# Performance work log

Measured on AMD Instinct MI355X. Metric: run time of the kernel, lower is better.

Reference implementation:

```python
import jax, jax.numpy as jnp
import numpy as np

L, H, C, D = 4, 4, 64, 64  # layers, heads, per-head out channels, embedding_dim
NEG_SLOPE = 0.2
LN_EPS = 1e-5

def layer_norm(x, g, b):
    mu = x.mean(-1, keepdims=True)
    var = ((x - mu) ** 2).mean(-1, keepdims=True)
    return (x - mu) * jax.lax.rsqrt(var + LN_EPS) * g + b

def setup_inputs() -> dict:
    key = jax.random.key(0)
    N, E = 20000, 320000
    ks = jax.random.split(key, 12)
    f = lambda k, shape: jax.random.normal(k, shape, jnp.float32) * 0.1
    return {
        "node_feats": jax.random.normal(ks[0], (N, D), jnp.float32),
        "edge_feats": jax.random.normal(ks[1], (E, D), jnp.float32),
        "edge_index": jax.random.randint(ks[2], (2, E), 0, N),
        "W_lin": f(ks[3], (L, D, H * C)),      # GAT node projection (bias=False)
        "W_edge": f(ks[4], (L, D, H * C)),     # GAT edge projection (bias=False)
        "att_src": f(ks[5], (L, H, C)),
        "att_dst": f(ks[6], (L, H, C)),
        "att_edge": f(ks[7], (L, H, C)),
        "bias_conv": f(ks[8], (L, D)),
        "ln_g": jnp.ones((L, D), jnp.float32),
        "ln_b": jnp.zeros((L, D), jnp.float32),
        "eW1": f(ks[9], (L, 3 * D, 3 * D)),
        "eb1": jnp.zeros((L, 3 * D), jnp.float32),
        "eln_g": jnp.ones((L, 3 * D), jnp.float32),
        "eln_b": jnp.zeros((L, 3 * D), jnp.float32),
        "eW2": f(ks[10], (L, 3 * D, D)),
        "eb2": jnp.zeros((L, D), jnp.float32),
    }

def reference(node_feats, edge_feats, edge_index, W_lin, W_edge, att_src,
              att_dst, att_edge, bias_conv, ln_g, ln_b, eW1, eb1, eln_g,
              eln_b, eW2, eb2):
    N = node_feats.shape[0]
    src, dst = edge_index[0], edge_index[1]
    for l in range(L):
        # --- GAT attention conv (concat=False: mean over heads) ---
        x = (node_feats @ W_lin[l]).reshape(N, H, C)
        e = (edge_feats @ W_edge[l]).reshape(-1, H, C)
        x_j, x_i = x[src], x[dst]                                  # [E,H,C]
        alpha = ((x_j * att_src[l]).sum(-1) + (x_i * att_dst[l]).sum(-1)
                 + (e * att_edge[l]).sum(-1))                      # [E,H]
        alpha = jax.nn.leaky_relu(alpha, NEG_SLOPE)
        amax = jax.ops.segment_max(alpha, dst, num_segments=N)
        alpha = jnp.exp(alpha - amax[dst])
        denom = jax.ops.segment_sum(alpha, dst, num_segments=N)
        alpha = alpha / (denom[dst] + 1e-16)
        out = jax.ops.segment_sum(x_j * alpha[..., None], dst, num_segments=N)
        out = out.mean(axis=1) + bias_conv[l]                      # [N,D]
        node_feats = layer_norm(out, ln_g[l], ln_b[l])
        # --- SparseEdgeUpdateLayer (residual=True) ---
        ni, nj = node_feats[src], node_feats[dst]
        h = jnp.concatenate([ni + nj, jnp.abs(ni - nj), edge_feats], axis=-1)
        h = jax.nn.relu(layer_norm(h @ eW1[l] + eb1[l], eln_g[l], eln_b[l]))
        edge_feats = h @ eW2[l] + eb2[l] + edge_feats
        # dropout is identity in eval mode
        if l < L - 1:
            node_feats = jax.nn.relu(node_feats)
    return node_feats, edge_feats
```

## Files before the change

kernel.cpp:

```cpp
#include <hip/hip_runtime.h>
#include <math.h>

#define NLAYERS 4
#define H 4
#define C 64
#define D 64
#define HC 256
#define D3 192
#define NEG 0.2f

typedef float f32x4 __attribute__((ext_vector_type(4)));
typedef short bf16x8 __attribute__((ext_vector_type(8)));
typedef unsigned short u16;

__device__ __forceinline__ u16 f2bf(float f) {
    unsigned u = __float_as_uint(f);
    u += 0x7FFFu + ((u >> 16) & 1u);
    return (u16)(u >> 16);
}
__device__ __forceinline__ float bf2f(u16 h) {
    return __uint_as_float((unsigned)h << 16);
}

__global__ void k_weffs(const float* __restrict__ W_edge, const float* __restrict__ att_edge,
                        const float* __restrict__ W_lin, const float* __restrict__ att_s,
                        const float* __restrict__ att_d,
                        float* __restrict__ weff, float* __restrict__ w_asd) {
    int l = blockIdx.x;
    const float* We = W_edge + (size_t)l * D * HC;
    const float* Wl = W_lin + (size_t)l * D * HC;
    const float* ae = att_edge + l * H * C;
    const float* as_ = att_s + l * H * C;
    const float* ad = att_d + l * H * C;
    int t = threadIdx.x;
    int d = t >> 2, h = t & 3;
    float se = 0.f, ss = 0.f, sd = 0.f;
    #pragma unroll
    for (int c = 0; c < C; ++c) {
        float we = We[d * HC + h * C + c];
        float wl = Wl[d * HC + h * C + c];
        se = fmaf(we, ae[h * C + c], se);
        ss = fmaf(wl, as_[h * C + c], ss);
        sd = fmaf(wl, ad[h * C + c], sd);
    }
    weff[l * HC + d * 4 + h] = se;
    w_asd[l * 512 + d * 8 + h] = ss;
    w_asd[l * 512 + d * 8 + 4 + h] = sd;
}

__global__ void k_cvtw(const float* __restrict__ W1, const float* __restrict__ W2,
                       u16* __restrict__ W1T, u16* __restrict__ W2T) {
    int i = blockIdx.x * 256 + threadIdx.x;
    if (i < NLAYERS * D3 * D3) {
        int l = i / (D3 * D3), r = i % (D3 * D3);
        int n = r / D3, k = r % D3;
        W1T[i] = f2bf(W1[l * D3 * D3 + k * D3 + n]);
    } else {
        int j = i - NLAYERS * D3 * D3;
        if (j < NLAYERS * D3 * D) {
            int l = j / (D3 * D), r = j % (D3 * D);
            int n = r / D3, k = r % D3;
            W2T[j] = f2bf(W2[l * D3 * D + k * D + n]);
        }
    }
}

__global__ void k_cvtwl(const float* __restrict__ W_lin,
                        u16* __restrict__ WTh, u16* __restrict__ WTl) {
    int i = blockIdx.x * 256 + threadIdx.x;
    if (i >= NLAYERS * HC * D) return;
    int l = i / (HC * D), r = i % (HC * D);
    int o = r / D, d = r % D;
    float v = W_lin[(size_t)l * D * HC + d * HC + o];
    u16 h = f2bf(v);
    WTh[i] = h;
    WTl[i] = f2bf(v - bf2f(h));
}

__global__ void k_hist(const int* __restrict__ dst, int* __restrict__ deg, int E) {
    int i = blockIdx.x * blockDim.x + threadIdx.x;
    if (i < E) atomicAdd(&deg[dst[i]], 1);
}

__global__ void k_scan(const int* __restrict__ deg, int* __restrict__ rowptr,
                       int* __restrict__ head, int N, int E) {
    __shared__ int lds[1024];
    int t = threadIdx.x;
    int chunk = (N + 1023) / 1024;
    int begin = t * chunk, end = min(begin + chunk, N);
    int sum = 0;
    for (int i = begin; i < end; ++i) sum += deg[i];
    lds[t] = sum;
    __syncthreads();
    for (int off = 1; off < 1024; off <<= 1) {
        int v = (t >= off) ? lds[t - off] : 0;
        __syncthreads();
        lds[t] += v;
        __syncthreads();
    }
    int running = (t == 0) ? 0 : lds[t - 1];
    for (int i = begin; i < end; ++i) {
        int dg = deg[i];
        rowptr[i] = running;
        head[i] = running;
        running += dg;
    }
    if (t == 0) rowptr[N] = E;
}

__global__ void k_scatter(const int* __restrict__ src, const int* __restrict__ dst,
                          int* __restrict__ head, int* __restrict__ csrpos,
                          int* __restrict__ perm_src, int E) {
    int i = blockIdx.x * blockDim.x + threadIdx.x;
    if (i < E) {
        int d = dst[i];
        int pos = atomicAdd(&head[d], 1);
        csrpos[i] = pos;
        perm_src[pos] = src[i];
    }
}

__global__ __launch_bounds__(256, 4) void k_nodeproj_mfma(
    const float* __restrict__ nf, const u16* __restrict__ WTh, const u16* __restrict__ WTl,
    const float* __restrict__ w_asd, float* __restrict__ x,
    float* __restrict__ a_src, float* __restrict__ a_dst, int N, int relu_in) {
    __shared__ __align__(16) u16 s_ah[32 * 72];
    __shared__ __align__(16) u16 s_al[32 * 72];
    __shared__ __align__(16) float s_nf[32][68];
    __shared__ __align__(16) float s_wasd[512];
    int tid = threadIdx.x;
    int w = tid >> 6, lane = tid & 63;
    int n0 = blockIdx.x << 5;

    if (tid < 128) *(float4*)&s_wasd[tid * 4] = *(const float4*)&w_asd[tid * 4];

    {
        int r = tid >> 3, c0 = (tid & 7) << 3;
        int n = n0 + r;
        float4 v0 = make_float4(0.f, 0.f, 0.f, 0.f), v1 = v0;
        if (n < N) {
            v0 = *(const float4*)&nf[(size_t)n * D + c0];
            v1 = *(const float4*)&nf[(size_t)n * D + c0 + 4];
        }
        if (relu_in) {
            v0.x = fmaxf(v0.x, 0.f); v0.y = fmaxf(v0.y, 0.f);
            v0.z = fmaxf(v0.z, 0.f); v0.w = fmaxf(v0.w, 0.f);
            v1.x = fmaxf(v1.x, 0.f); v1.y = fmaxf(v1.y, 0.f);
            v1.z = fmaxf(v1.z, 0.f); v1.w = fmaxf(v1.w, 0.f);
        }
        *(float4*)&s_nf[r][c0] = v0;
        *(float4*)&s_nf[r][c0 + 4] = v1;
        float vv[8] = {v0.x, v0.y, v0.z, v0.w, v1.x, v1.y, v1.z, v1.w};
        bf16x8 hv, lv;
        #pragma unroll
        for (int j = 0; j < 8; ++j) {
            u16 h = f2bf(vv[j]);
            hv[j] = (short)h;
            lv[j] = (short)f2bf(vv[j] - bf2f(h));
        }
        *(bf16x8*)&s_ah[r * 72 + c0] = hv;
        *(bf16x8*)&s_al[r * 72 + c0] = lv;
    }
    __syncthreads();

    int m16 = lane & 15, quad = lane >> 4, kq = quad * 8;
    f32x4 acc[2][4];
    #pragma unroll
    for (int mt = 0; mt < 2; ++mt)
        #pragma unroll
        for (int nt = 0; nt < 4; ++nt) {
            acc[mt][nt][0] = 0.f; acc[mt][nt][1] = 0.f;
            acc[mt][nt][2] = 0.f; acc[mt][nt][3] = 0.f;
        }
    #pragma unroll
    for (int ks = 0; ks < 2; ++ks) {
        int ko = ks * 32 + kq;
        bf16x8 ah0 = *(const bf16x8*)&s_ah[m16 * 72 + ko];
        bf16x8 ah1 = *(const bf16x8*)&s_ah[(16 + m16) * 72 + ko];
        bf16x8 al0 = *(const bf16x8*)&s_al[m16 * 72 + ko];
        bf16x8 al1 = *(const bf16x8*)&s_al[(16 + m16) * 72 + ko];
        #pragma unroll
        for (int nt = 0; nt < 4; ++nt) {
            int col = w * 64 + nt * 16 + m16;
            bf16x8 bh = *(const bf16x8*)&WTh[col * D + ko];
            bf16x8 bl = *(const bf16x8*)&WTl[col * D + ko];
            acc[0][nt] = __builtin_amdgcn_mfma_f32_16x16x32_bf16(ah0, bh, acc[0][nt], 0, 0, 0);
            acc[0][nt] = __builtin_amdgcn_mfma_f32_16x16x32_bf16(al0, bh, acc[0][nt], 0, 0, 0);
            acc[0][nt] = __builtin_amdgcn_mfma_f32_16x16x32_bf16(ah0, bl, acc[0][nt], 0, 0, 0);
            acc[1][nt] = __builtin_amdgcn_mfma_f32_16x16x32_bf16(ah1, bh, acc[1][nt], 0, 0, 0);
            acc[1][nt] = __builtin_amdgcn_mfma_f32_16x16x32_bf16(al1, bh, acc[1][nt], 0, 0, 0);
            acc[1][nt] = __builtin_amdgcn_mfma_f32_16x16x32_bf16(ah1, bl, acc[1][nt], 0, 0, 0);
        }
    }
    #pragma unroll
    for (int mt = 0; mt < 2; ++mt) {
        #pragma unroll
        for (int nt = 0; nt < 4; ++nt) {
            int col = w * 64 + nt * 16 + m16;
            #pragma unroll
            for (int r = 0; r < 4; ++r) {
                int n = n0 + mt * 16 + quad * 4 + r;
                if (n < N) x[(size_t)n * HC + col] = acc[mt][nt][r];
            }
        }
    }

    {
        int nloc = tid >> 3, o = tid & 7;
        float s = 0.f;
        #pragma unroll
        for (int d = 0; d < 64; ++d)
            s = fmaf(s_nf[nloc][d], s_wasd[d * 8 + o], s);
        int n = n0 + nloc;
        if (n < N) {
            if (o < 4) a_src[n * 4 + o] = s;
            else       a_dst[n * 4 + (o - 4)] = s;
        }
    }
}

__global__ void k_alpha(const float* __restrict__ ef, const float* __restrict__ weff,
                        const int* __restrict__ src, const int* __restrict__ dst,
                        const float* __restrict__ a_src, const float* __restrict__ a_dst,
                        const int* __restrict__ csrpos, float* __restrict__ alpha_csr, int E) {
    int wave = (int)((blockIdx.x * blockDim.x + threadIdx.x) >> 6);
    int lane = threadIdx.x & 63;
    int sub = lane >> 4, li = lane & 15;
    int e = wave * 4 + sub;
    if (e >= E) return;
    float4 efv = *(const float4*)&ef[(size_t)e * D + li * 4];
    float4 w0 = *(const float4*)&weff[(li * 4 + 0) * 4];
    float4 w1 = *(const float4*)&weff[(li * 4 + 1) * 4];
    float4 w2 = *(const float4*)&weff[(li * 4 + 2) * 4];
    float4 w3 = *(const float4*)&weff[(li * 4 + 3) * 4];
    float p0 = efv.x * w0.x + efv.y * w1.x + efv.z * w2.x + efv.w * w3.x;
    float p1 = efv.x * w0.y + efv.y * w1.y + efv.z * w2.y + efv.w * w3.y;
    float p2 = efv.x * w0.z + efv.y * w1.z + efv.z * w2.z + efv.w * w3.z;
    float p3 = efv.x * w0.w + efv.y * w1.w + efv.z * w2.w + efv.w * w3.w;
    #pragma unroll
    for (int off = 1; off < 16; off <<= 1) {
        p0 += __shfl_xor(p0, off);
        p1 += __shfl_xor(p1, off);
        p2 += __shfl_xor(p2, off);
        p3 += __shfl_xor(p3, off);
    }
    if (li < 4) {
        float p = (li == 0) ? p0 : (li == 1) ? p1 : (li == 2) ? p2 : p3;
        int s = src[e], dd = dst[e];
        float a = p + a_src[s * 4 + li] + a_dst[dd * 4 + li];
        a = (a > 0.f) ? a : NEG * a;
        alpha_csr[(size_t)csrpos[e] * 4 + li] = a;
    }
}

__global__ void k_gat(const float* __restrict__ x, float* __restrict__ alpha_csr,
                      const int* __restrict__ rowptr, const int* __restrict__ perm_src,
                      const float* __restrict__ bias, const float* __restrict__ g,
                      const float* __restrict__ b, float* __restrict__ nf_ln,
                      float* __restrict__ out2, int N) {
    int n = (int)((blockIdx.x * blockDim.x + threadIdx.x) >> 6);
    int lane = threadIdx.x & 63;
    if (n >= N) return;
    int s = rowptr[n], e = rowptr[n + 1];
    int deg = e - s;
    float m0 = -1e30f, m1 = -1e30f, m2 = -1e30f, m3 = -1e30f;
    for (int i = lane; i < deg; i += 64) {
        const float4 a = *(const float4*)&alpha_csr[(size_t)(s + i) * 4];
        m0 = fmaxf(m0, a.x); m1 = fmaxf(m1, a.y);
        m2 = fmaxf(m2, a.z); m3 = fmaxf(m3, a.w);
    }
    #pragma unroll
    for (int off = 32; off; off >>= 1) {
        m0 = fmaxf(m0, __shfl_xor(m0, off)); m1 = fmaxf(m1, __shfl_xor(m1, off));
        m2 = fmaxf(m2, __shfl_xor(m2, off)); m3 = fmaxf(m3, __shfl_xor(m3, off));
    }
    float d0 = 0.f, d1 = 0.f, d2 = 0.f, d3 = 0.f;
    for (int i = lane; i < deg; i += 64) {
        float4 a = *(const float4*)&alpha_csr[(size_t)(s + i) * 4];
        a.x = expf(a.x - m0); a.y = expf(a.y - m1);
        a.z = expf(a.z - m2); a.w = expf(a.w - m3);
        *(float4*)&alpha_csr[(size_t)(s + i) * 4] = a;
        d0 += a.x; d1 += a.y; d2 += a.z; d3 += a.w;
    }
    #pragma unroll
    for (int off = 32; off; off >>= 1) {
        d0 += __shfl_xor(d0, off); d1 += __shfl_xor(d1, off);
        d2 += __shfl_xor(d2, off); d3 += __shfl_xor(d3, off);
    }
    float i0 = 0.25f / (d0 + 1e-16f), i1 = 0.25f / (d1 + 1e-16f);
    float i2 = 0.25f / (d2 + 1e-16f), i3 = 0.25f / (d3 + 1e-16f);
    float ac0 = 0.f, ac1 = 0.f, ac2 = 0.f, ac3 = 0.f;
    int j = 0;
    for (; j + 3 < deg; j += 4) {
        const float4 a0 = *(const float4*)&alpha_csr[(size_t)(s + j + 0) * 4];
        const float4 a1 = *(const float4*)&alpha_csr[(size_t)(s + j + 1) * 4];
        const float4 a2 = *(const float4*)&alpha_csr[(size_t)(s + j + 2) * 4];
        const float4 a3 = *(const float4*)&alpha_csr[(size_t)(s + j + 3) * 4];
        int s0 = perm_src[s + j + 0], s1 = perm_src[s + j + 1];
        int s2 = perm_src[s + j + 2], s3 = perm_src[s + j + 3];
        const float* x0 = x + (size_t)s0 * HC;
        const float* x1 = x + (size_t)s1 * HC;
        const float* x2 = x + (size_t)s2 * HC;
        const float* x3 = x + (size_t)s3 * HC;
        ac0 += a0.x * i0 * x0[lane] + a0.y * i1 * x0[64 + lane]
             + a0.z * i2 * x0[128 + lane] + a0.w * i3 * x0[192 + lane];
        ac1 += a1.x * i0 * x1[lane] + a1.y * i1 * x1[64 + lane]
             + a1.z * i2 * x1[128 + lane] + a1.w * i3 * x1[192 + lane];
        ac2 += a2.x * i0 * x2[lane] + a2.y * i1 * x2[64 + lane]
             + a2.z * i2 * x2[128 + lane] + a2.w * i3 * x2[192 + lane];
        ac3 += a3.x * i0 * x3[lane] + a3.y * i1 * x3[64 + lane]
             + a3.z * i2 * x3[128 + lane] + a3.w * i3 * x3[192 + lane];
    }
    for (; j < deg; ++j) {
        const float4 a = *(const float4*)&alpha_csr[(size_t)(s + j) * 4];
        int sidx = perm_src[s + j];
        const float* xr = x + (size_t)sidx * HC;
        ac0 += a.x * i0 * xr[lane] + a.y * i1 * xr[64 + lane]
             + a.z * i2 * xr[128 + lane] + a.w * i3 * xr[192 + lane];
    }
    float acc = (ac0 + ac1) + (ac2 + ac3);
    float v = acc + bias[lane];
    float sm = v;
    #pragma unroll
    for (int off = 32; off; off >>= 1) sm += __shfl_xor(sm, off);
    float mu = sm * (1.f / 64.f);
    float dv = v - mu;
    float q = dv * dv;
    #pragma unroll
    for (int off = 32; off; off >>= 1) q += __shfl_xor(q, off);
    float rstd = rsqrtf(q * (1.f / 64.f) + 1e-5f);
    float r = dv * rstd * g[lane] + b[lane];
    nf_ln[(size_t)n * D + lane] = r;
    if (out2) out2[(size_t)n * D + lane] = r;
}

__global__ __launch_bounds__(256, 5) void k_edgemlp_mfma(
    const float* __restrict__ nf, const float* __restrict__ ef_in,
    const int* __restrict__ src, const int* __restrict__ dst,
    const u16* __restrict__ W1T, const float* __restrict__ b1,
    const float* __restrict__ lg, const float* __restrict__ lb,
    const u16* __restrict__ W2T, const float* __restrict__ b2,
    float* __restrict__ ef_out, int E) {
    __shared__ __align__(16) u16 A1[64 * 200];
    __shared__ float ps[4][64], pq[4][64];
    int tid = threadIdx.x;
    int w = tid >> 6, lane = tid & 63;
    int e0 = blockIdx.x * 64;
    int ebase = e0 + w * 16;

    int idxv = 0;
    if (lane < 16)      idxv = src[min(ebase + lane, E - 1)];
    else if (lane < 32) idxv = dst[min(ebase + lane - 16, E - 1)];

    {
        int half = lane >> 5;
        int c2 = (lane & 31) << 1;
        #pragma unroll
        for (int it = 0; it < 8; ++it) {
            int eloc = 2 * it + half;
            int ge = ebase + eloc;
            int sA = __shfl(idxv, eloc);
            int dA = __shfl(idxv, 16 + eloc);
            float2 za = make_float2(0.f, 0.f), zb = za, zf = za;
            if (ge < E) {
                za = *(const float2*)&nf[(size_t)sA * D + c2];
                zb = *(const float2*)&nf[(size_t)dA * D + c2];
                zf = *(const float2*)&ef_in[(size_t)ge * D + c2];
            }
            unsigned su = (unsigned)f2bf(za.x + zb.x) | ((unsigned)f2bf(za.y + zb.y) << 16);
            unsigned du = (unsigned)f2bf(fabsf(za.x - zb.x)) | ((unsigned)f2bf(fabsf(za.y - zb.y)) << 16);
            unsigned fu = (unsigned)f2bf(zf.x) | ((unsigned)f2bf(zf.y) << 16);
            int row = w * 16 + eloc;
            *(unsigned*)&A1[row * 200 + c2]       = su;
            *(unsigned*)&A1[row * 200 + 64 + c2]  = du;
            *(unsigned*)&A1[row * 200 + 128 + c2] = fu;
        }
    }
    __syncthreads();

    int m16 = lane & 15, quad = lane >> 4, kq = quad * 8;
    f32x4 acc[4][3];
    #pragma unroll
    for (int nt = 0; nt < 3; ++nt) {
        float bv = b1[w * 48 + nt * 16 + m16];
        #pragma unroll
        for (int mt = 0; mt < 4; ++mt) {
            acc[mt][nt][0] = bv; acc[mt][nt][1] = bv;
            acc[mt][nt][2] = bv; acc[mt][nt][3] = bv;
        }
    }
    #pragma unroll
    for (int ks = 0; ks < 6; ++ks) {
        int ko = ks * 32 + kq;
        bf16x8 af0 = *(const bf16x8*)&A1[(0  + m16) * 200 + ko];
        bf16x8 af1 = *(const bf16x8*)&A1[(16 + m16) * 200 + ko];
        bf16x8 af2 = *(const bf16x8*)&A1[(32 + m16) * 200 + ko];
        bf16x8 af3 = *(const bf16x8*)&A1[(48 + m16) * 200 + ko];
        #pragma unroll
        for (int nt = 0; nt < 3; ++nt) {
            bf16x8 bfr = *(const bf16x8*)&W1T[(w * 48 + nt * 16 + m16) * D3 + ko];
            acc[0][nt] = __builtin_amdgcn_mfma_f32_16x16x32_bf16(af0, bfr, acc[0][nt], 0, 0, 0);
            acc[1][nt] = __builtin_amdgcn_mfma_f32_16x16x32_bf16(af1, bfr, acc[1][nt], 0, 0, 0);
            acc[2][nt] = __builtin_amdgcn_mfma_f32_16x16x32_bf16(af2, bfr, acc[2][nt], 0, 0, 0);
            acc[3][nt] = __builtin_amdgcn_mfma_f32_16x16x32_bf16(af3, bfr, acc[3][nt], 0, 0, 0);
        }
    }

    #pragma unroll
    for (int mt = 0; mt < 4; ++mt) {
        float s8[4], q8[4];
        #pragma unroll
        for (int r = 0; r < 4; ++r) {
            float v0 = acc[mt][0][r], v1 = acc[mt][1][r], v2 = acc[mt][2][r];
            s8[r] = v0 + v1 + v2;
            q8[r] = v0 * v0 + v1 * v1 + v2 * v2;
        }
        #pragma unroll
        for (int off = 1; off < 16; off <<= 1) {
            #pragma unroll
            for (int r = 0; r < 4; ++r) {
                s8[r] += __shfl_xor(s8[r], off);
                q8[r] += __shfl_xor(q8[r], off);
            }
        }
        if (m16 == 0) {
            #pragma unroll
            for (int r = 0; r < 4; ++r) {
                int row = mt * 16 + quad * 4 + r;
                ps[w][row] = s8[r];
                pq[w][row] = q8[r];
            }
        }
    }
    __syncthreads();

    float mu_l, rs_l;
    {
        float s = ps[0][lane] + ps[1][lane] + ps[2][lane] + ps[3][lane];
        float q = pq[0][lane] + pq[1][lane] + pq[2][lane] + pq[3][lane];
        mu_l = s * (1.f / 192.f);
        rs_l = rsqrtf(q * (1.f / 192.f) - mu_l * mu_l + 1e-5f);
    }

    {
        float gg0 = lg[w * 48 + 0 * 16 + m16], bb0 = lb[w * 48 + 0 * 16 + m16];
        float gg1 = lg[w * 48 + 1 * 16 + m16], bb1 = lb[w * 48 + 1 * 16 + m16];
        float gg2 = lg[w * 48 + 2 * 16 + m16], bb2 = lb[w * 48 + 2 * 16 + m16];
        #pragma unroll
        for (int mt = 0; mt < 4; ++mt) {
            #pragma unroll
            for (int r = 0; r < 4; ++r) {
                int row = mt * 16 + quad * 4 + r;
                float mu = __shfl(mu_l, row);
                float rstd = __shfl(rs_l, row);
                float v0 = (acc[mt][0][r] - mu) * rstd * gg0 + bb0;
                float v1 = (acc[mt][1][r] - mu) * rstd * gg1 + bb1;
                float v2 = (acc[mt][2][r] - mu) * rstd * gg2 + bb2;
                A1[row * 200 + w * 48 + 0 * 16 + m16] = f2bf(fmaxf(v0, 0.f));
                A1[row * 200 + w * 48 + 1 * 16 + m16] = f2bf(fmaxf(v1, 0.f));
                A1[row * 200 + w * 48 + 2 * 16 + m16] = f2bf(fmaxf(v2, 0.f));
            }
        }
    }
    __syncthreads();

    int col2 = w * 16 + m16;
    f32x4 acc2[4];
    {
        float bv = b2[col2];
        #pragma unroll
        for (int mt = 0; mt < 4; ++mt) {
            acc2[mt][0] = bv; acc2[mt][1] = bv; acc2[mt][2] = bv; acc2[mt][3] = bv;
        }
    }
    #pragma unroll
    for (int ks = 0; ks < 6; ++ks) {
        int ko = ks * 32 + kq;
        bf16x8 b2f = *(const bf16x8*)&W2T[col2 * D3 + ko];
        bf16x8 a2f0 = *(const bf16x8*)&A1[(0  + m16) * 200 + ko];
        bf16x8 a2f1 = *(const bf16x8*)&A1[(16 + m16) * 200 + ko];
        bf16x8 a2f2 = *(const bf16x8*)&A1[(32 + m16) * 200 + ko];
        bf16x8 a2f3 = *(const bf16x8*)&A1[(48 + m16) * 200 + ko];
        acc2[0] = __builtin_amdgcn_mfma_f32_16x16x32_bf16(a2f0, b2f, acc2[0], 0, 0, 0);
        acc2[1] = __builtin_amdgcn_mfma_f32_16x16x32_bf16(a2f1, b2f, acc2[1], 0, 0, 0);
        acc2[2] = __builtin_amdgcn_mfma_f32_16x16x32_bf16(a2f2, b2f, acc2[2], 0, 0, 0);
        acc2[3] = __builtin_amdgcn_mfma_f32_16x16x32_bf16(a2f3, b2f, acc2[3], 0, 0, 0);
    }
    #pragma unroll
    for (int mt = 0; mt < 4; ++mt) {
        int row0 = mt * 16 + quad * 4;
        #pragma unroll
        for (int r = 0; r < 4; ++r) {
            int ge = e0 + row0 + r;
            if (ge < E) {
                size_t o = (size_t)ge * D + col2;
                ef_out[o] = acc2[mt][r] + ef_in[o];
            }
        }
    }
}

extern "C" void kernel_launch(void* const* d_in, const int* in_sizes, int n_in,
                              void* d_out, int out_size, void* d_ws, size_t ws_size,
                              hipStream_t stream) {
    const float* nf_in0   = (const float*)d_in[0];
    const float* ef_in0   = (const float*)d_in[1];
    const int*   eidx     = (const int*)d_in[2];
    const float* W_lin    = (const float*)d_in[3];
    const float* W_edge   = (const float*)d_in[4];
    const float* att_src  = (const float*)d_in[5];
    const float* att_dst  = (const float*)d_in[6];
    const float* att_edge = (const float*)d_in[7];
    const float* biasc    = (const float*)d_in[8];
    const float* ln_g     = (const float*)d_in[9];
    const float* ln_b     = (const float*)d_in[10];
    const float* eW1      = (const float*)d_in[11];
    const float* eb1      = (const float*)d_in[12];
    const float* eln_g    = (const float*)d_in[13];
    const float* eln_b    = (const float*)d_in[14];
    const float* eW2      = (const float*)d_in[15];
    const float* eb2      = (const float*)d_in[16];

    int N = in_sizes[0] / D;
    int E = in_sizes[1] / D;
    const int* srcp = eidx;
    const int* dstp = eidx + E;

    float* ws        = (float*)d_ws;
    float* x         = ws;
    float* alpha_csr = x + (size_t)N * HC;
    float* a_src     = alpha_csr + (size_t)E * H;
    float* a_dst     = a_src + (size_t)N * H;
    float* nf_ln     = a_dst + (size_t)N * H;
    float* weff      = nf_ln + (size_t)N * D;
    float* w_asd     = weff + NLAYERS * HC;
    u16*   W1T       = (u16*)(w_asd + NLAYERS * 512);
    u16*   W2T       = W1T + (size_t)NLAYERS * D3 * D3;
    u16*   WLh       = W2T + (size_t)NLAYERS * D3 * D;
    u16*   WLl       = WLh + (size_t)NLAYERS * HC * D;
    int*   rowptr    = (int*)(WLl + (size_t)NLAYERS * HC * D);
    int*   head      = rowptr + (N + 1);
    int*   csrpos    = head + N;
    int*   perm_src  = csrpos + (size_t)E;

    float* out_nf = (float*)d_out;
    float* out_ef = out_nf + (size_t)N * D;

    {
        int total = NLAYERS * D3 * D3 + NLAYERS * D3 * D;
        k_cvtw<<<(total + 255) / 256, 256, 0, stream>>>(eW1, eW2, W1T, W2T);
        k_cvtwl<<<(NLAYERS * HC * D + 255) / 256, 256, 0, stream>>>(W_lin, WLh, WLl);
        k_weffs<<<NLAYERS, 256, 0, stream>>>(W_edge, att_edge, W_lin, att_src, att_dst,
                                             weff, w_asd);
        hipMemsetAsync(head, 0, (size_t)N * sizeof(int), stream);
        k_hist<<<(E + 255) / 256, 256, 0, stream>>>(dstp, head, E);
        k_scan<<<1, 1024, 0, stream>>>(head, rowptr, head, N, E);
        k_scatter<<<(E + 255) / 256, 256, 0, stream>>>(srcp, dstp, head, csrpos, perm_src, E);
    }

    for (int l = 0; l < NLAYERS; ++l) {
        const float* nf_cur = (l == 0) ? nf_in0 : nf_ln;
        const float* ef_cur = (l == 0) ? ef_in0 : out_ef;
        int relu_in = (l > 0) ? 1 : 0;

        k_nodeproj_mfma<<<(N + 31) / 32, 256, 0, stream>>>(
            nf_cur, WLh + (size_t)l * HC * D, WLl + (size_t)l * HC * D,
            w_asd + (size_t)l * 512, x, a_src, a_dst, N, relu_in);
        k_alpha<<<(E + 15) / 16, 256, 0, stream>>>(ef_cur, weff + (size_t)l * HC, srcp, dstp,
                                                   a_src, a_dst, csrpos, alpha_csr, E);
        k_gat<<<(N + 3) / 4, 256, 0, stream>>>(x, alpha_csr, rowptr, perm_src,
                                               biasc + l * D, ln_g + l * D, ln_b + l * D,
                                               nf_ln, (l == NLAYERS - 1) ? out_nf : nullptr, N);
        k_edgemlp_mfma<<<(E + 63) / 64, 256, 0, stream>>>(nf_ln, ef_cur, srcp, dstp,
                                                          W1T + (size_t)l * D3 * D3, eb1 + l * D3,
                                                          eln_g + l * D3, eln_b + l * D3,
                                                          W2T + (size_t)l * D3 * D, eb2 + l * D,
                                                          out_ef, E);
    }
}
```

Baseline: 1.038 ms.

## Fuse next-layer edge attention projection into edge MLP epilogue

The edge MLP kernel's epilogue now stages the freshly computed edge features in shared memory and takes their dot product with the next layer's folded edge-attention weights (weff). It writes a per-edge, per-head partial alpha. For layers after the first, the alpha kernel becomes a lightweight elementwise pass that adds the source and destination terms and applies leaky-relu. This removes a full re-read of the E×64 edge features per layer, at the cost of extra shared-memory work, a barrier in the edge MLP, and an extra workspace buffer.

```diff
diff --git a/kernel.cpp b/kernel.cpp
--- a/kernel.cpp
+++ b/kernel.cpp
@@ -251,6 +251,18 @@
         a = (a > 0.f) ? a : NEG * a;
         alpha_csr[(size_t)csrpos[e] * 4 + li] = a;
     }
+}
+
+__global__ void k_alpha_lite(const float* __restrict__ palpha,
+                             const int* __restrict__ src, const int* __restrict__ dst,
+                             const float* __restrict__ a_src, const float* __restrict__ a_dst,
+                             const int* __restrict__ csrpos, float* __restrict__ alpha_csr, int E) {
+    int i = blockIdx.x * 256 + threadIdx.x;
+    if (i >= E * 4) return;
+    int e = i >> 2, h = i & 3;
+    float a = palpha[i] + a_src[src[e] * 4 + h] + a_dst[dst[e] * 4 + h];
+    a = (a > 0.f) ? a : NEG * a;
+    alpha_csr[(size_t)csrpos[e] * 4 + h] = a;
 }
 
 __global__ void k_gat(const float* __restrict__ x, float* __restrict__ alpha_csr,
@@ -340,7 +352,8 @@
     const u16* __restrict__ W1T, const float* __restrict__ b1,
     const float* __restrict__ lg, const float* __restrict__ lb,
     const u16* __restrict__ W2T, const float* __restrict__ b2,
-    float* __restrict__ ef_out, int E) {
+    float* __restrict__ ef_out, const float* __restrict__ weffN,
+    float* __restrict__ palpha, int E) {
     __shared__ __align__(16) u16 A1[64 * 200];
     __shared__ float ps[4][64], pq[4][64];
     int tid = threadIdx.x;
@@ -492,11 +505,35 @@
         #pragma unroll
         for (int r = 0; r < 4; ++r) {
             int ge = e0 + row0 + r;
+            float v = 0.f;
             if (ge < E) {
                 size_t o = (size_t)ge * D + col2;
-                ef_out[o] = acc2[mt][r] + ef_in[o];
+                v = acc2[mt][r] + ef_in[o];
+                ef_out[o] = v;
             }
-        }
+            acc2[mt][r] = v;
+        }
+    }
+
+    if (palpha) {
+        __syncthreads();
+        float* A1f = (float*)A1;
+        #pragma unroll
+        for (int mt = 0; mt < 4; ++mt) {
+            #pragma unroll
+            for (int r = 0; r < 4; ++r)
+                A1f[(mt * 16 + quad * 4 + r) * 68 + col2] = acc2[mt][r];
+        }
+        float* wst = &ps[0][0];
+        if (tid < 64) *(float4*)&wst[tid * 4] = *(const float4*)&weffN[tid * 4];
+        __syncthreads();
+        int e = tid >> 2, h = tid & 3;
+        int ge = e0 + e;
+        float p = 0.f;
+        #pragma unroll
+        for (int d = 0; d < 64; ++d)
+            p = fmaf(A1f[e * 68 + d], wst[d * 4 + h], p);
+        if (ge < E) palpha[(size_t)ge * 4 + h] = p;
     }
 }
 
@@ -542,6 +579,7 @@
     int*   head      = rowptr + (N + 1);
     int*   csrpos    = head + N;
     int*   perm_src  = csrpos + (size_t)E;
+    float* palpha    = (float*)(perm_src + (size_t)E);
 
     float* out_nf = (float*)d_out;
     float* out_ef = out_nf + (size_t)N * D;
@@ -566,15 +604,24 @@
         k_nodeproj_mfma<<<(N + 31) / 32, 256, 0, stream>>>(
             nf_cur, WLh + (size_t)l * HC * D, WLl + (size_t)l * HC * D,
             w_asd + (size_t)l * 512, x, a_src, a_dst, N, relu_in);
-        k_alpha<<<(E + 15) / 16, 256, 0, stream>>>(ef_cur, weff + (size_t)l * HC, srcp, dstp,
-                                                   a_src, a_dst, csrpos, alpha_csr, E);
+        if (l == 0) {
+            k_alpha<<<(E + 15) / 16, 256, 0, stream>>>(ef_cur, weff + (size_t)l * HC,
+                                                       srcp, dstp, a_src, a_dst,
+                                                       csrpos, alpha_csr, E);
+        } else {
+            k_alpha_lite<<<(E * 4 + 255) / 256, 256, 0, stream>>>(palpha, srcp, dstp,
+                                                                  a_src, a_dst,
+                                                                  csrpos, alpha_csr, E);
+        }
         k_gat<<<(N + 3) / 4, 256, 0, stream>>>(x, alpha_csr, rowptr, perm_src,
                                                biasc + l * D, ln_g + l * D, ln_b + l * D,
                                                nf_ln, (l == NLAYERS - 1) ? out_nf : nullptr, N);
+        const float* weffN = (l < NLAYERS - 1) ? (weff + (size_t)(l + 1) * HC) : nullptr;
+        float* pout = (l < NLAYERS - 1) ? palpha : nullptr;
         k_edgemlp_mfma<<<(E + 63) / 64, 256, 0, stream>>>(nf_ln, ef_cur, srcp, dstp,
                                                           W1T + (size_t)l * D3 * D3, eb1 + l * D3,
                                                           eln_g + l * D3, eln_b + l * D3,
                                                           W2T + (size_t)l * D3 * D, eb2 + l * D,
-                                                          out_ef, E);
-    }
-}
+                                                          out_ef, weffN, pout, E);
+    }
+}
```

New measurement: 1.007 ms. 1.03x faster.
